# Optimization experiments

Hardware: AMD Instinct MI355X
Metric: run time of the kernel (lower is better)

## Reference

```python
import jax, jax.numpy as jnp
import numpy as np

N = 125000   # lattice cells (50^3)
K = 26       # max neighbors (3D Moore neighborhood)
D = 32       # state_size
STEPS = 3    # CNF integration steps (explicit Euler)


def setup_inputs() -> dict:
    key = jax.random.key(0)
    ks = jax.random.split(key, 12)
    s = 0.1  # small init so tanh stays in its linear-ish regime
    return {
        "full_lattice_states": jax.random.normal(ks[0], (N, D), jnp.float32),
        "neighbor_indices": jax.random.randint(ks[1], (N, K), 0, N, jnp.int32),
        "tier_ids": jax.random.randint(ks[2], (N, K), 0, 3, jnp.int32),
        # local expert (SimpleLinear): [cur ; local_agg] -> D
        "W_loc": jax.random.normal(ks[3], (2 * D, D), jnp.float32) * s,
        "b_loc": jnp.zeros((D,), jnp.float32),
        # functional expert (HybridGNN): per-neighbor message + combine
        "W_msg": jax.random.normal(ks[4], (D, D), jnp.float32) * s,
        "b_msg": jnp.zeros((D,), jnp.float32),
        "W_fun": jax.random.normal(ks[5], (2 * D, D), jnp.float32) * s,
        "b_fun": jnp.zeros((D,), jnp.float32),
        # distant expert (LightweightCNF): ODE drift on [x ; distant_agg]
        "W_cnf": jax.random.normal(ks[6], (2 * D, D), jnp.float32) * s,
        "b_cnf": jnp.zeros((D,), jnp.float32),
        # gating network: [cur ; local_agg ; func_agg ; dist_agg] -> 3 experts
        "W_gate": jax.random.normal(ks[7], (4 * D, 3), jnp.float32) * s,
        "b_gate": jnp.zeros((3,), jnp.float32),
    }


def reference(full_lattice_states, neighbor_indices, tier_ids,
              W_loc, b_loc, W_msg, b_msg, W_fun, b_fun,
              W_cnf, b_cnf, W_gate, b_gate):
    cur = full_lattice_states                      # [N, D]
    nbr = full_lattice_states[neighbor_indices]    # [N, K, D] gather (irregular access)

    def tier_mean(x, t):
        # masked mean over neighbors belonging to tier t
        m = (tier_ids == t)[..., None].astype(x.dtype)           # [N, K, 1]
        return (x * m).sum(axis=1) / jnp.maximum(m.sum(axis=1), 1.0)  # [N, D]

    local_agg = tier_mean(nbr, 0)   # [N, D]
    func_agg = tier_mean(nbr, 1)    # [N, D]
    dist_agg = tier_mean(nbr, 2)    # [N, D]

    # local expert: single linear on [cur ; local_agg]
    local_out = jnp.tanh(jnp.concatenate([cur, local_agg], -1) @ W_loc + b_loc)

    # functional expert: GNN message passing over functional-tier neighbors
    msgs = jnp.tanh(nbr @ W_msg + b_msg)           # [N, K, D]
    func_msg = tier_mean(msgs, 1)                  # [N, D]
    func_out = jnp.tanh(jnp.concatenate([cur, func_msg], -1) @ W_fun + b_fun)

    # distant expert: lightweight CNF, explicit Euler conditioned on dist_agg
    dt = 1.0 / STEPS
    x = cur
    for _ in range(STEPS):
        x = x + dt * jnp.tanh(jnp.concatenate([x, dist_agg], -1) @ W_cnf + b_cnf)
    dist_out = x

    # gating: adaptive weighting of the 3 experts
    gate_in = jnp.concatenate([cur, local_agg, func_agg, dist_agg], -1)  # [N, 4D]
    w = jax.nn.softmax(gate_in @ W_gate + b_gate, axis=-1)               # [N, 3]

    out = (w[:, 0:1] * local_out + w[:, 1:2] * func_out + w[:, 2:3] * dist_out)
    return out
```

## Files before the change

### kernel.cpp

```cpp
#include <hip/hip_runtime.h>
#include <hip/hip_bf16.h>
#include <math.h>

#define NCELL 125000
#define KNBR  26
#define D     32
#define MC    64

#define SXE (127.0f/7.0f)
#define SXD (7.0f/127.0f)
#define SMD (1.0f/127.0f)

__device__ __forceinline__ float fast_tanh(float x) {
    float e = __expf(2.0f * x);
    return 1.0f - 2.0f / (e + 1.0f);
}
__device__ __forceinline__ float bf2f(unsigned int h) {
    return __uint_as_float(h << 16);
}

__global__ void __launch_bounds__(256) msg_kernel(
    const float* __restrict__ X, const float* __restrict__ Wm,
    const float* __restrict__ bm,
    signed char* __restrict__ Xq, signed char* __restrict__ Mq)
{
    __shared__ float sX[256];
    int t = blockIdx.x * 256 + threadIdx.x;
    float v = X[t];
    sX[threadIdx.x] = v;
    float xc = fminf(fmaxf(v, -7.f), 7.f);
    Xq[t] = (signed char)__float2int_rn(xc * SXE);
    __syncthreads();
    int d = t & 31;
    int base = threadIdx.x & ~31;
    float acc = bm[d];
#pragma unroll
    for (int j = 0; j < D; ++j)
        acc = fmaf(sX[base + j], Wm[j * D + d], acc);
    Mq[t] = (signed char)__float2int_rn(fast_tanh(acc) * 127.0f);
}

__global__ void __launch_bounds__(256) agg_kernel(
    const signed char* __restrict__ Xq, const signed char* __restrict__ Mq,
    const int* __restrict__ nbr, const int* __restrict__ tier,
    __hip_bfloat16* __restrict__ aggs)
{
    __shared__ int sPack[8 * KNBR];
    int tid = threadIdx.x;
    int blockCell = blockIdx.x * 8;
    if (tid < 8 * KNBR) {
        int g = blockCell * KNBR + tid;
        sPack[tid] = (nbr[g] << 2) | tier[g];
    }
    __syncthreads();

    int grp = tid >> 5, d = tid & 31;
    int c = blockCell + grp;
    int sAll = 0, s0 = 0, s1 = 0, sm = 0, n0 = 0, n1 = 0;
#pragma unroll
    for (int k = 0; k < KNBR; ++k) {
        int pk = sPack[grp * KNBR + k];
        int tt = pk & 3;
        int j  = pk >> 2;
        int q = Xq[j * D + d];
        bool t0 = (tt == 0), t1 = (tt == 1);
        sAll += q;
        s0 += t0 ? q : 0;   n0 += t0;
        s1 += t1 ? q : 0;   n1 += t1;
        if (t1) sm += Mq[j * D + d];
    }
    int s2 = sAll - s0 - s1;
    float n2 = (float)(KNBR - n0 - n1);
    __hip_bfloat16* a = aggs + (size_t)c * 4 * D + d;
    a[0 * D] = __float2bfloat16((float)s0 * SXD / fmaxf((float)n0, 1.f));
    a[1 * D] = __float2bfloat16((float)s1 * SXD / fmaxf((float)n1, 1.f));
    a[2 * D] = __float2bfloat16((float)s2 * SXD / fmaxf(n2, 1.f));
    a[3 * D] = __float2bfloat16((float)sm * SMD / fmaxf((float)n1, 1.f));
}

__global__ void __launch_bounds__(256) moe_kernel(
    const float* __restrict__ X, const unsigned int* __restrict__ aggs,
    const float* __restrict__ Wl, const float* __restrict__ bl,
    const float* __restrict__ Wf, const float* __restrict__ bfv,
    const float* __restrict__ Wc, const float* __restrict__ bc,
    const float* __restrict__ Wg, const float* __restrict__ bg,
    float* __restrict__ out)
{
    __shared__ float sX[MC * 32];
    __shared__ unsigned int sA[MC * 64];
    int tid  = threadIdx.x;
    int base = blockIdx.x * MC;
    int cells = NCELL - base; if (cells > MC) cells = MC;

    const float4* gX = (const float4*)(X + (size_t)base * 32);
#pragma unroll
    for (int k = 0; k < 2; ++k) {
        int q4 = tid + k * 256;
        if (q4 * 4 < cells * 32) {
            float4 v = gX[q4];
            int g = q4 * 4, cc = g >> 5, j = g & 31, s = cc & 31;
            sX[cc * 32 + ((j + 0) ^ s)] = v.x;
            sX[cc * 32 + ((j + 1) ^ s)] = v.y;
            sX[cc * 32 + ((j + 2) ^ s)] = v.z;
            sX[cc * 32 + ((j + 3) ^ s)] = v.w;
        }
    }
    const uint4* gA = (const uint4*)(aggs + (size_t)base * 64);
#pragma unroll
    for (int k = 0; k < 4; ++k) {
        int q4 = tid + k * 256;
        if (q4 * 4 < cells * 64) {
            uint4 v = gA[q4];
            int g = q4 * 4, cc = g >> 6, p = g & 63, s = cc & 31;
            sA[cc * 64 + ((p + 0) ^ s)] = v.x;
            sA[cc * 64 + ((p + 1) ^ s)] = v.y;
            sA[cc * 64 + ((p + 2) ^ s)] = v.z;
            sA[cc * 64 + ((p + 3) ^ s)] = v.w;
        }
    }
    __syncthreads();

    int role = tid >> 6, cc = tid & 63;
    int s = cc & 31;
    bool act = (cc < cells);
    float res[32];
    float w0 = 0.f, w1 = 0.f, w2 = 0.f;

    if (act && role == 0) {
        float g0 = bg[0], g1 = bg[1], g2 = bg[2];
#pragma unroll 8
        for (int j = 0; j < 32; ++j) {
            float v = sX[cc * 32 + (j ^ s)];
            g0 = fmaf(v, Wg[j*3+0], g0); g1 = fmaf(v, Wg[j*3+1], g1); g2 = fmaf(v, Wg[j*3+2], g2);
        }
#pragma unroll 8
        for (int p = 0; p < 48; ++p) {
            unsigned int dw = sA[cc * 64 + (p ^ s)];
            float vlo = bf2f(dw & 0xffffu), vhi = bf2f(dw >> 16);
            int r = 32 + p * 2;
            g0 = fmaf(vlo, Wg[r*3+0], g0); g1 = fmaf(vlo, Wg[r*3+1], g1); g2 = fmaf(vlo, Wg[r*3+2], g2);
            g0 = fmaf(vhi, Wg[(r+1)*3+0], g0); g1 = fmaf(vhi, Wg[(r+1)*3+1], g1); g2 = fmaf(vhi, Wg[(r+1)*3+2], g2);
        }
        float mx = fmaxf(g0, fmaxf(g1, g2));
        float e0 = __expf(g0 - mx), e1 = __expf(g1 - mx), e2 = __expf(g2 - mx);
        float inv = 1.f / (e0 + e1 + e2);
        w0 = e0 * inv; w1 = e1 * inv; w2 = e2 * inv;
    } else if (act && role == 1) {
        float gc[32];
#pragma unroll
        for (int d0 = 0; d0 < 32; ++d0) gc[d0] = bc[d0];
#pragma unroll 4
        for (int p = 0; p < 16; ++p) {
            unsigned int dw = sA[cc * 64 + ((32 + p) ^ s)];
            float vlo = bf2f(dw & 0xffffu), vhi = bf2f(dw >> 16);
            int j = 32 + p * 2;
#pragma unroll
            for (int d0 = 0; d0 < 32; ++d0) gc[d0] = fmaf(vlo, Wc[j * 32 + d0], gc[d0]);
#pragma unroll
            for (int d0 = 0; d0 < 32; ++d0) gc[d0] = fmaf(vhi, Wc[(j + 1) * 32 + d0], gc[d0]);
        }
        float xx[32];
#pragma unroll
        for (int d0 = 0; d0 < 32; ++d0) xx[d0] = sX[cc * 32 + (d0 ^ s)];
        const float dt = 1.0f / 3.0f;
#pragma unroll 1
        for (int st = 0; st < 3; ++st) {
            float a2[32];
#pragma unroll
            for (int d0 = 0; d0 < 32; ++d0) a2[d0] = gc[d0];
#pragma unroll 8
            for (int j = 0; j < 32; ++j) {
                float v = xx[j];
#pragma unroll
                for (int d0 = 0; d0 < 32; ++d0) a2[d0] = fmaf(v, Wc[j * 32 + d0], a2[d0]);
            }
#pragma unroll
            for (int d0 = 0; d0 < 32; ++d0) xx[d0] += dt * fast_tanh(a2[d0]);
        }
#pragma unroll
        for (int d0 = 0; d0 < 32; ++d0) res[d0] = xx[d0];
    } else if (act && role == 2) {
#pragma unroll
        for (int d0 = 0; d0 < 32; ++d0) res[d0] = bl[d0];
#pragma unroll 8
        for (int j = 0; j < 32; ++j) {
            float v = sX[cc * 32 + (j ^ s)];
#pragma unroll
            for (int d0 = 0; d0 < 32; ++d0) res[d0] = fmaf(v, Wl[j * 32 + d0], res[d0]);
        }
#pragma unroll 4
        for (int p = 0; p < 16; ++p) {
            unsigned int dw = sA[cc * 64 + (p ^ s)];
            float vlo = bf2f(dw & 0xffffu), vhi = bf2f(dw >> 16);
            int j = 32 + p * 2;
#pragma unroll
            for (int d0 = 0; d0 < 32; ++d0) res[d0] = fmaf(vlo, Wl[j * 32 + d0], res[d0]);
#pragma unroll
            for (int d0 = 0; d0 < 32; ++d0) res[d0] = fmaf(vhi, Wl[(j + 1) * 32 + d0], res[d0]);
        }
#pragma unroll
        for (int d0 = 0; d0 < 32; ++d0) res[d0] = fast_tanh(res[d0]);
    } else if (act && role == 3) {
#pragma unroll
        for (int d0 = 0; d0 < 32; ++d0) res[d0] = bfv[d0];
#pragma unroll 8
        for (int j = 0; j < 32; ++j) {
            float v = sX[cc * 32 + (j ^ s)];
#pragma unroll
            for (int d0 = 0; d0 < 32; ++d0) res[d0] = fmaf(v, Wf[j * 32 + d0], res[d0]);
        }
#pragma unroll 4
        for (int p = 0; p < 16; ++p) {
            unsigned int dw = sA[cc * 64 + ((48 + p) ^ s)];
            float vlo = bf2f(dw & 0xffffu), vhi = bf2f(dw >> 16);
            int j = 32 + p * 2;
#pragma unroll
            for (int d0 = 0; d0 < 32; ++d0) res[d0] = fmaf(vlo, Wf[j * 32 + d0], res[d0]);
#pragma unroll
            for (int d0 = 0; d0 < 32; ++d0) res[d0] = fmaf(vhi, Wf[(j + 1) * 32 + d0], res[d0]);
        }
#pragma unroll
        for (int d0 = 0; d0 < 32; ++d0) res[d0] = fast_tanh(res[d0]);
    }
    __syncthreads();

    float* sFr = (float*)sA;
    float* sCr = sFr + MC * 32;
    if (act) {
        if (role == 2) {
#pragma unroll
            for (int d0 = 0; d0 < 32; ++d0) sX[cc * 32 + (d0 ^ s)] = res[d0];
        } else if (role == 3) {
#pragma unroll
            for (int d0 = 0; d0 < 32; ++d0) sFr[cc * 32 + (d0 ^ s)] = res[d0];
        } else if (role == 1) {
#pragma unroll
            for (int d0 = 0; d0 < 32; ++d0) sCr[cc * 32 + (d0 ^ s)] = res[d0];
        }
    }
    __syncthreads();

    if (act && role == 0) {
        float o[32];
#pragma unroll
        for (int d0 = 0; d0 < 32; ++d0) {
            float lo = sX [cc * 32 + (d0 ^ s)];
            float fo = sFr[cc * 32 + (d0 ^ s)];
            float xo = sCr[cc * 32 + (d0 ^ s)];
            o[d0] = w0 * lo + w1 * fo + w2 * xo;
        }
#pragma unroll
        for (int d0 = 0; d0 < 32; ++d0) sX[cc * 32 + (d0 ^ s)] = o[d0];
    }
    __syncthreads();

    float4* gO = (float4*)(out + (size_t)base * 32);
#pragma unroll
    for (int k = 0; k < 2; ++k) {
        int q4 = tid + k * 256;
        if (q4 * 4 < cells * 32) {
            int g = q4 * 4, cc2 = g >> 5, j = g & 31, s2 = cc2 & 31;
            float4 v;
            v.x = sX[cc2 * 32 + ((j + 0) ^ s2)];
            v.y = sX[cc2 * 32 + ((j + 1) ^ s2)];
            v.z = sX[cc2 * 32 + ((j + 2) ^ s2)];
            v.w = sX[cc2 * 32 + ((j + 3) ^ s2)];
            gO[q4] = v;
        }
    }
}

extern "C" void kernel_launch(void* const* d_in, const int* in_sizes, int n_in,
                              void* d_out, int out_size, void* d_ws, size_t ws_size,
                              hipStream_t stream)
{
    const float* X    = (const float*)d_in[0];
    const int*   nbr  = (const int*)  d_in[1];
    const int*   tier = (const int*)  d_in[2];
    const float* Wl   = (const float*)d_in[3];
    const float* bl   = (const float*)d_in[4];
    const float* Wm   = (const float*)d_in[5];
    const float* bm   = (const float*)d_in[6];
    const float* Wf   = (const float*)d_in[7];
    const float* bf   = (const float*)d_in[8];
    const float* Wc   = (const float*)d_in[9];
    const float* bc   = (const float*)d_in[10];
    const float* Wg   = (const float*)d_in[11];
    const float* bg   = (const float*)d_in[12];
    float* out = (float*)d_out;

    const size_t ND = (size_t)NCELL * D;
    signed char* Xq = (signed char*)d_ws;
    signed char* Mq = Xq + ND;
    __hip_bfloat16* aggs = (__hip_bfloat16*)(Mq + ND);

    dim3 blk(256);
    msg_kernel<<<dim3(ND / 256), blk, 0, stream>>>(X, Wm, bm, Xq, Mq);
    agg_kernel<<<dim3(NCELL / 8), blk, 0, stream>>>(Xq, Mq, nbr, tier, aggs);
    moe_kernel<<<dim3((NCELL + MC - 1) / MC), blk, 0, stream>>>(
        X, (const unsigned int*)aggs, Wl, bl, Wf, bf, Wc, bc, Wg, bg, out);
}
```

Measured before the change: 250.3 us.

## Interleave quantized state and message into one gather buffer, add nontemporal accesses

The int8 quantized state and int8 message for each cell and dim are packed into a single 16-bit word. The aggregation gather then issues one load per neighbor instead of a separate conditional load from the message array. Streaming reads of the neighbor and tier indices, the aggregate writes, and the final output now use nontemporal loads and stores to reduce cache pollution. The CNF loop reuses the res array as its accumulator to cut register pressure. The cost is that non-functional-tier neighbors also pull message bytes, and bf16 conversion is now done by hand.

```diff
diff --git a/kernel.cpp b/kernel.cpp
--- a/kernel.cpp
+++ b/kernel.cpp
@@ -11,6 +11,9 @@
 #define SXD (7.0f/127.0f)
 #define SMD (1.0f/127.0f)
 
+typedef unsigned int uint4v __attribute__((ext_vector_type(4)));
+typedef float float4v __attribute__((ext_vector_type(4)));
+
 __device__ __forceinline__ float fast_tanh(float x) {
     float e = __expf(2.0f * x);
     return 1.0f - 2.0f / (e + 1.0f);
@@ -18,18 +21,20 @@
 __device__ __forceinline__ float bf2f(unsigned int h) {
     return __uint_as_float(h << 16);
 }
+__device__ __forceinline__ unsigned short f2bf(float f) {
+    unsigned int u = __float_as_uint(f);
+    u += 0x7fffu + ((u >> 16) & 1u);
+    return (unsigned short)(u >> 16);
+}
 
 __global__ void __launch_bounds__(256) msg_kernel(
     const float* __restrict__ X, const float* __restrict__ Wm,
-    const float* __restrict__ bm,
-    signed char* __restrict__ Xq, signed char* __restrict__ Mq)
+    const float* __restrict__ bm, unsigned short* __restrict__ XM)
 {
     __shared__ float sX[256];
     int t = blockIdx.x * 256 + threadIdx.x;
     float v = X[t];
     sX[threadIdx.x] = v;
-    float xc = fminf(fmaxf(v, -7.f), 7.f);
-    Xq[t] = (signed char)__float2int_rn(xc * SXE);
     __syncthreads();
     int d = t & 31;
     int base = threadIdx.x & ~31;
@@ -37,20 +42,24 @@
 #pragma unroll
     for (int j = 0; j < D; ++j)
         acc = fmaf(sX[base + j], Wm[j * D + d], acc);
-    Mq[t] = (signed char)__float2int_rn(fast_tanh(acc) * 127.0f);
+    int xq = __float2int_rn(fminf(fmaxf(v, -7.f), 7.f) * SXE);
+    int mq = __float2int_rn(fast_tanh(acc) * 127.0f);
+    XM[t] = (unsigned short)(((mq & 0xff) << 8) | (xq & 0xff));
 }
 
 __global__ void __launch_bounds__(256) agg_kernel(
-    const signed char* __restrict__ Xq, const signed char* __restrict__ Mq,
+    const unsigned short* __restrict__ XM,
     const int* __restrict__ nbr, const int* __restrict__ tier,
-    __hip_bfloat16* __restrict__ aggs)
+    unsigned short* __restrict__ aggs)
 {
     __shared__ int sPack[8 * KNBR];
     int tid = threadIdx.x;
     int blockCell = blockIdx.x * 8;
     if (tid < 8 * KNBR) {
         int g = blockCell * KNBR + tid;
-        sPack[tid] = (nbr[g] << 2) | tier[g];
+        int jj = __builtin_nontemporal_load(&nbr[g]);
+        int tt = __builtin_nontemporal_load(&tier[g]);
+        sPack[tid] = (jj << 2) | tt;
     }
     __syncthreads();
 
@@ -62,20 +71,22 @@
         int pk = sPack[grp * KNBR + k];
         int tt = pk & 3;
         int j  = pk >> 2;
-        int q = Xq[j * D + d];
+        unsigned short v = XM[j * D + d];
+        int x = (int)(signed char)(v & 0xff);
+        int m = (int)(signed char)(v >> 8);
         bool t0 = (tt == 0), t1 = (tt == 1);
-        sAll += q;
-        s0 += t0 ? q : 0;   n0 += t0;
-        s1 += t1 ? q : 0;   n1 += t1;
-        if (t1) sm += Mq[j * D + d];
+        sAll += x;
+        s0 += t0 ? x : 0;   n0 += t0;
+        s1 += t1 ? x : 0;   n1 += t1;
+        sm += t1 ? m : 0;
     }
     int s2 = sAll - s0 - s1;
     float n2 = (float)(KNBR - n0 - n1);
-    __hip_bfloat16* a = aggs + (size_t)c * 4 * D + d;
-    a[0 * D] = __float2bfloat16((float)s0 * SXD / fmaxf((float)n0, 1.f));
-    a[1 * D] = __float2bfloat16((float)s1 * SXD / fmaxf((float)n1, 1.f));
-    a[2 * D] = __float2bfloat16((float)s2 * SXD / fmaxf(n2, 1.f));
-    a[3 * D] = __float2bfloat16((float)sm * SMD / fmaxf((float)n1, 1.f));
+    unsigned short* a = aggs + (size_t)c * 4 * D + d;
+    __builtin_nontemporal_store(f2bf((float)s0 * SXD / fmaxf((float)n0, 1.f)), a + 0 * D);
+    __builtin_nontemporal_store(f2bf((float)s1 * SXD / fmaxf((float)n1, 1.f)), a + 1 * D);
+    __builtin_nontemporal_store(f2bf((float)s2 * SXD / fmaxf(n2, 1.f)),        a + 2 * D);
+    __builtin_nontemporal_store(f2bf((float)sm * SMD / fmaxf((float)n1, 1.f)), a + 3 * D);
 }
 
 __global__ void __launch_bounds__(256) moe_kernel(
@@ -105,12 +116,12 @@
             sX[cc * 32 + ((j + 3) ^ s)] = v.w;
         }
     }
-    const uint4* gA = (const uint4*)(aggs + (size_t)base * 64);
+    const uint4v* gA = (const uint4v*)(aggs + (size_t)base * 64);
 #pragma unroll
     for (int k = 0; k < 4; ++k) {
         int q4 = tid + k * 256;
         if (q4 * 4 < cells * 64) {
-            uint4 v = gA[q4];
+            uint4v v = __builtin_nontemporal_load(&gA[q4]);
             int g = q4 * 4, cc = g >> 6, p = g & 63, s = cc & 31;
             sA[cc * 64 + ((p + 0) ^ s)] = v.x;
             sA[cc * 64 + ((p + 1) ^ s)] = v.y;
@@ -146,7 +157,7 @@
         float inv = 1.f / (e0 + e1 + e2);
         w0 = e0 * inv; w1 = e1 * inv; w2 = e2 * inv;
     } else if (act && role == 1) {
-        float gc[32];
+        float gc[32], xx[32];
 #pragma unroll
         for (int d0 = 0; d0 < 32; ++d0) gc[d0] = bc[d0];
 #pragma unroll 4
@@ -159,23 +170,21 @@
 #pragma unroll
             for (int d0 = 0; d0 < 32; ++d0) gc[d0] = fmaf(vhi, Wc[(j + 1) * 32 + d0], gc[d0]);
         }
-        float xx[32];
 #pragma unroll
         for (int d0 = 0; d0 < 32; ++d0) xx[d0] = sX[cc * 32 + (d0 ^ s)];
         const float dt = 1.0f / 3.0f;
 #pragma unroll 1
         for (int st = 0; st < 3; ++st) {
-            float a2[32];
-#pragma unroll
-            for (int d0 = 0; d0 < 32; ++d0) a2[d0] = gc[d0];
+#pragma unroll
+            for (int d0 = 0; d0 < 32; ++d0) res[d0] = gc[d0];
 #pragma unroll 8
             for (int j = 0; j < 32; ++j) {
                 float v = xx[j];
 #pragma unroll
-                for (int d0 = 0; d0 < 32; ++d0) a2[d0] = fmaf(v, Wc[j * 32 + d0], a2[d0]);
+                for (int d0 = 0; d0 < 32; ++d0) res[d0] = fmaf(v, Wc[j * 32 + d0], res[d0]);
             }
 #pragma unroll
-            for (int d0 = 0; d0 < 32; ++d0) xx[d0] += dt * fast_tanh(a2[d0]);
+            for (int d0 = 0; d0 < 32; ++d0) xx[d0] += dt * fast_tanh(res[d0]);
         }
 #pragma unroll
         for (int d0 = 0; d0 < 32; ++d0) res[d0] = xx[d0];
@@ -254,18 +263,18 @@
     }
     __syncthreads();
 
-    float4* gO = (float4*)(out + (size_t)base * 32);
+    float4v* gO = (float4v*)(out + (size_t)base * 32);
 #pragma unroll
     for (int k = 0; k < 2; ++k) {
         int q4 = tid + k * 256;
         if (q4 * 4 < cells * 32) {
             int g = q4 * 4, cc2 = g >> 5, j = g & 31, s2 = cc2 & 31;
-            float4 v;
+            float4v v;
             v.x = sX[cc2 * 32 + ((j + 0) ^ s2)];
             v.y = sX[cc2 * 32 + ((j + 1) ^ s2)];
             v.z = sX[cc2 * 32 + ((j + 2) ^ s2)];
             v.w = sX[cc2 * 32 + ((j + 3) ^ s2)];
-            gO[q4] = v;
+            __builtin_nontemporal_store(v, &gO[q4]);
         }
     }
 }
@@ -290,13 +299,12 @@
     float* out = (float*)d_out;
 
     const size_t ND = (size_t)NCELL * D;
-    signed char* Xq = (signed char*)d_ws;
-    signed char* Mq = Xq + ND;
-    __hip_bfloat16* aggs = (__hip_bfloat16*)(Mq + ND);
+    unsigned short* XM = (unsigned short*)d_ws;
+    unsigned short* aggs = XM + ND;
 
     dim3 blk(256);
-    msg_kernel<<<dim3(ND / 256), blk, 0, stream>>>(X, Wm, bm, Xq, Mq);
-    agg_kernel<<<dim3(NCELL / 8), blk, 0, stream>>>(Xq, Mq, nbr, tier, aggs);
+    msg_kernel<<<dim3(ND / 256), blk, 0, stream>>>(X, Wm, bm, XM);
+    agg_kernel<<<dim3(NCELL / 8), blk, 0, stream>>>(XM, nbr, tier, aggs);
     moe_kernel<<<dim3((NCELL + MC - 1) / MC), blk, 0, stream>>>(
         X, (const unsigned int*)aggs, Wl, bl, Wf, bf, Wc, bc, Wg, bg, out);
 }
```

Result: faster. 226.5 us (-9.5%).
